# Optimization experiments

Hardware: AMD Instinct MI355X
Metric: run time of the kernel (lower is better)

## Reference

```python
import jax, jax.numpy as jnp
import numpy as np

N_CLASSES = 256
PER_CLASS = 128
N_SUPPORT = 5
N_QUERY = PER_CLASS - N_SUPPORT  # 123
N_VIEW = 2
D = 384
N = N_CLASSES * PER_CLASS  # 32768


def setup_inputs() -> dict:
    key = jax.random.key(0)
    k1, k2 = jax.random.split(key, 2)
    reps = jax.random.normal(k1, (N, N_VIEW, D), dtype=jnp.float32)
    # block-sorted labels: class c occupies rows [c*PER_CLASS, (c+1)*PER_CLASS)
    labels = (jnp.arange(N, dtype=jnp.int32) // PER_CLASS).astype(jnp.int32)
    return {"reps": reps, "labels": labels}


def reference(reps, labels):
    # labels are block-sorted per class, so the original's
    # labels.eq(c).nonzero()[:n_support] / [n_support:] gathers are static reshapes.
    reps_r = reps.reshape(N_CLASSES, PER_CLASS, N_VIEW, D)
    # class-mean prototypes over the support set: [C, V, D]
    prototypes = reps_r[:, :N_SUPPORT].mean(axis=1)
    # query samples: [C*N_QUERY, V, D]
    queries = reps_r[:, N_SUPPORT:].reshape(N_CLASSES * N_QUERY, N_VIEW, D)

    x2 = jnp.sum(queries * queries, axis=-1)            # [n, V]
    y2 = jnp.sum(prototypes * prototypes, axis=-1)      # [m, V]
    xy = jnp.einsum('nvd,mvd->nmv', queries, prototypes)  # [n, m, V]
    dists = x2[:, None, :] + y2[None, :, :] - 2.0 * xy

    # log_softmax over the prototype (class) axis
    log_p_y = jax.nn.log_softmax(-dists, axis=1)
    log_p_y = log_p_y.reshape(N_CLASSES, N_QUERY, N_CLASSES, N_VIEW)

    # gather the true-class log-prob for each query / view
    cls = jnp.arange(N_CLASSES)
    correct = log_p_y[cls, :, cls, :]  # [C, N_QUERY, V]
    loss = -correct.mean()
    return loss
```

## Files before the change

### kernel.cpp

```cpp
#include <hip/hip_runtime.h>
#include <hip/hip_bf16.h>
#include <math.h>

#define NCLS 256
#define PER_CLASS 128
#define NSUP 5
#define NQRY 123
#define NVIEW 2
#define DD 384
#define NQ_TOT (NCLS * NQRY)
#define BM 128
#define BK 32
#define NKT (DD / BK)
#define QS 40

typedef __attribute__((ext_vector_type(8))) short short8;
typedef __attribute__((ext_vector_type(4))) float floatx4;

union FragU { uint4 u; short8 s; };
union PkU { __hip_bfloat162 b2; unsigned int u; };

__device__ __forceinline__ unsigned int cvt2bf(float lo, float hi) {
    PkU p;
    p.b2 = __float22bfloat162_rn(make_float2(lo, hi));
    return p.u;
}

#define BARRIER() asm volatile("s_waitcnt lgkmcnt(0)\n\ts_barrier" ::: "memory")

__global__ __launch_bounds__(384) void proto_kernel(const float* __restrict__ reps,
                                                    ushort* __restrict__ pbf,
                                                    float* __restrict__ y2) {
    __shared__ float wp[6];
    const int b = blockIdx.x;
    const int c = b & 255, v = b >> 8;
    const int d = threadIdx.x;
    const float* p = reps + ((size_t)(c * PER_CLASS) * NVIEW + v) * DD + d;
    float s = 0.f;
#pragma unroll
    for (int k = 0; k < NSUP; ++k) s += p[(size_t)k * NVIEW * DD];
    s *= 0.2f;
    __hip_bfloat16 h = __float2bfloat16(s);
    pbf[(size_t)b * DD + d] = *reinterpret_cast<ushort*>(&h);
    float q = s * s;
#pragma unroll
    for (int o = 1; o < 64; o <<= 1) q += __shfl_xor(q, o);
    if ((d & 63) == 0) wp[d >> 6] = q;
    __syncthreads();
    if (d == 0) y2[b] = wp[0] + wp[1] + wp[2] + wp[3] + wp[4] + wp[5];
}

__global__ __launch_bounds__(256, 2) void main_kernel(const float* __restrict__ reps,
                                                      const ushort* __restrict__ pbf,
                                                      const float* __restrict__ y2g,
                                                      float* __restrict__ out) {
    __shared__ ushort q_lds[2][BM * QS];
    __shared__ ushort p_lds[2][NCLS * QS];
    __shared__ float pmx[BM][2];
    __shared__ float pse[BM][2];
    __shared__ float wred[8];

    const int t = threadIdx.x;
    const int v = blockIdx.y;
    const int q0 = blockIdx.x * BM;
    const int wave = t >> 6;
    const int lane = t & 63;
    const int col = lane & 15;
    const int quad = lane >> 4;
    const int wm = wave >> 1;
    const int wn = wave & 1;

    const int sq = t >> 1;
    const int h16 = (t & 1) * 16;
    const int nq = q0 + sq;
    const float* qsrc = reps +
        (size_t)((nq / NQRY) * PER_CLASS + NSUP + (nq % NQRY)) * (NVIEW * DD) + v * DD + h16;
    const ushort* psrc = pbf + (size_t)(v * NCLS + t) * DD;

    floatx4 acc[4][8];
#pragma unroll
    for (int mt = 0; mt < 4; ++mt)
#pragma unroll
        for (int nt = 0; nt < 8; ++nt) acc[mt][nt] = (floatx4)0.f;

    float4 qf[4];
    uint4 pl[4];

#define LOADT(kt)                                                                  \
    do {                                                                           \
        _Pragma("unroll") for (int i = 0; i < 4; ++i)                              \
            qf[i] = *(const float4*)(qsrc + (kt) * BK + i * 4);                    \
        _Pragma("unroll") for (int i = 0; i < 4; ++i)                              \
            pl[i] = *((const uint4*)(psrc + (kt) * BK) + i);                       \
    } while (0)

#define STAGE(b)                                                                   \
    do {                                                                           \
        uint4 qw0, qw1;                                                            \
        qw0.x = cvt2bf(qf[0].x, qf[0].y); qw0.y = cvt2bf(qf[0].z, qf[0].w);        \
        qw0.z = cvt2bf(qf[1].x, qf[1].y); qw0.w = cvt2bf(qf[1].z, qf[1].w);        \
        qw1.x = cvt2bf(qf[2].x, qf[2].y); qw1.y = cvt2bf(qf[2].z, qf[2].w);        \
        qw1.z = cvt2bf(qf[3].x, qf[3].y); qw1.w = cvt2bf(qf[3].z, qf[3].w);        \
        *(uint4*)&q_lds[b][sq * QS + h16] = qw0;                                   \
        *(uint4*)&q_lds[b][sq * QS + h16 + 8] = qw1;                               \
        _Pragma("unroll") for (int i = 0; i < 4; ++i)                              \
            *(uint4*)&p_lds[b][t * QS + i * 8] = pl[i];                            \
    } while (0)

#define COMPUTE(b)                                                                 \
    do {                                                                           \
        short8 af[4];                                                              \
        _Pragma("unroll") for (int mt = 0; mt < 4; ++mt) {                         \
            FragU f;                                                               \
            f.u = *(const uint4*)&q_lds[b][(wm * 64 + mt * 16 + col) * QS + quad * 8]; \
            af[mt] = f.s;                                                          \
        }                                                                          \
        _Pragma("unroll") for (int nt = 0; nt < 8; ++nt) {                         \
            FragU bb;                                                              \
            bb.u = *(const uint4*)&p_lds[b][(wn * 128 + nt * 16 + col) * QS + quad * 8]; \
            _Pragma("unroll") for (int mt = 0; mt < 4; ++mt)                       \
                acc[mt][nt] = __builtin_amdgcn_mfma_f32_16x16x32_bf16(af[mt], bb.s, acc[mt][nt], 0, 0, 0); \
        }                                                                          \
    } while (0)

    LOADT(0);
    STAGE(0);
    LOADT(1);
    BARRIER();
#pragma unroll
    for (int kt = 0; kt < NKT; ++kt) {
        COMPUTE(kt & 1);
        if (kt < NKT - 1) {
            STAGE((kt + 1) & 1);
            if (kt < NKT - 2) LOADT(kt + 2);
            BARRIER();
        }
    }

    float y2c[8];
#pragma unroll
    for (int nt = 0; nt < 8; ++nt) y2c[nt] = y2g[v * NCLS + wn * 128 + nt * 16 + col];

    float corr = 0.f;
#pragma unroll
    for (int mt = 0; mt < 4; ++mt) {
#pragma unroll
        for (int r = 0; r < 4; ++r) {
            const int qloc = wm * 64 + mt * 16 + quad * 4 + r;
            const int n = q0 + qloc;
            const int cn = n / NQRY;
            float s[8];
            float mx = -1e30f;
#pragma unroll
            for (int nt = 0; nt < 8; ++nt) {
                s[nt] = 2.f * acc[mt][nt][r] - y2c[nt];
                mx = fmaxf(mx, s[nt]);
                if (cn == wn * 128 + nt * 16 + col) corr += s[nt];
            }
#pragma unroll
            for (int o = 1; o < 16; o <<= 1) mx = fmaxf(mx, __shfl_xor(mx, o));
            float e = 0.f;
#pragma unroll
            for (int nt = 0; nt < 8; ++nt) e += __expf(s[nt] - mx);
#pragma unroll
            for (int o = 1; o < 16; o <<= 1) e += __shfl_xor(e, o);
            if (col == 0) { pmx[qloc][wn] = mx; pse[qloc][wn] = e; }
        }
    }
#pragma unroll
    for (int o = 1; o < 64; o <<= 1) corr += __shfl_xor(corr, o);
    if (lane == 0) wred[wave] = corr;
    __syncthreads();

    float lval = 0.f;
    if (t < BM) {
        float m0 = pmx[t][0], m1 = pmx[t][1];
        float M = fmaxf(m0, m1);
        float E = pse[t][0] * __expf(m0 - M) + pse[t][1] * __expf(m1 - M);
        lval = M + __logf(E);
    }
#pragma unroll
    for (int o = 1; o < 64; o <<= 1) lval += __shfl_xor(lval, o);
    if (lane == 0) wred[4 + wave] = lval;
    __syncthreads();

    if (t == 0) {
        float tot = (wred[4] + wred[5] + wred[6] + wred[7]) -
                    (wred[0] + wred[1] + wred[2] + wred[3]);
        atomicAdd(out, tot * (1.f / (float)(NQ_TOT * NVIEW)));
    }
}

extern "C" void kernel_launch(void* const* d_in, const int* in_sizes, int n_in,
                              void* d_out, int out_size, void* d_ws, size_t ws_size,
                              hipStream_t stream) {
    const float* reps = (const float*)d_in[0];
    float* ws = (float*)d_ws;
    ushort* pbf = (ushort*)ws;
    float* y2 = (float*)(pbf + NVIEW * NCLS * DD);
    float* out = (float*)d_out;

    hipMemsetAsync(out, 0, sizeof(float), stream);
    proto_kernel<<<dim3(NVIEW * NCLS), dim3(DD), 0, stream>>>(reps, pbf, y2);
    main_kernel<<<dim3(NQ_TOT / BM, NVIEW), dim3(256), 0, stream>>>(reps, pbf, y2, out);
}
```

Before: 164.9 us.

## Load prototype tiles via global_load_lds with XOR swizzle and deeper Q prefetch

Prototype bf16 tiles now go straight from global memory into LDS through global_load_lds, skipping the register round trip. They use an XOR-swizzled unpadded layout to avoid bank conflicts on MFMA fragment reads. Query loads are double-buffered in registers two tiles ahead, with explicit vmcnt waits. The separate memset is folded into the prototype kernel to remove a launch. The cost is more complex synchronisation and tighter correctness requirements on the swizzle and wait counts.

```diff
diff --git a/kernel.cpp b/kernel.cpp
--- a/kernel.cpp
+++ b/kernel.cpp
@@ -13,6 +13,7 @@
 #define BK 32
 #define NKT (DD / BK)
 #define QS 40
+#define PS 32
 
 typedef __attribute__((ext_vector_type(8))) short short8;
 typedef __attribute__((ext_vector_type(4))) float floatx4;
@@ -26,15 +27,24 @@
     return p.u;
 }
 
+__device__ __forceinline__ void gll16(const ushort* g, ushort* l) {
+    __builtin_amdgcn_global_load_lds(
+        (const __attribute__((address_space(1))) unsigned int*)g,
+        (__attribute__((address_space(3))) unsigned int*)l, 16, 0, 0);
+}
+
 #define BARRIER() asm volatile("s_waitcnt lgkmcnt(0)\n\ts_barrier" ::: "memory")
+#define WAITVM(n) asm volatile("s_waitcnt vmcnt(" #n ")" ::: "memory")
 
 __global__ __launch_bounds__(384) void proto_kernel(const float* __restrict__ reps,
                                                     ushort* __restrict__ pbf,
-                                                    float* __restrict__ y2) {
+                                                    float* __restrict__ y2,
+                                                    float* __restrict__ out) {
     __shared__ float wp[6];
     const int b = blockIdx.x;
     const int c = b & 255, v = b >> 8;
     const int d = threadIdx.x;
+    if (b == 0 && d == 0) out[0] = 0.f;
     const float* p = reps + ((size_t)(c * PER_CLASS) * NVIEW + v) * DD + d;
     float s = 0.f;
 #pragma unroll
@@ -55,7 +65,7 @@
                                                       const float* __restrict__ y2g,
                                                       float* __restrict__ out) {
     __shared__ ushort q_lds[2][BM * QS];
-    __shared__ ushort p_lds[2][NCLS * QS];
+    __shared__ ushort p_lds[2][NCLS * PS];
     __shared__ float pmx[BM][2];
     __shared__ float pse[BM][2];
     __shared__ float wred[8];
@@ -75,7 +85,15 @@
     const int nq = q0 + sq;
     const float* qsrc = reps +
         (size_t)((nq / NQRY) * PER_CLASS + NSUP + (nq % NQRY)) * (NVIEW * DD) + v * DD + h16;
-    const ushort* psrc = pbf + (size_t)(v * NCLS + t) * DD;
+
+    const ushort* psrc = pbf + (size_t)(v * NCLS + wave * 64 + (lane >> 2)) * DD
+                             + (((lane & 3) ^ ((lane >> 3) & 3)) << 3);
+
+    const int sP = (col >> 1) & 3;
+    int boff[8];
+#pragma unroll
+    for (int nt = 0; nt < 8; ++nt)
+        boff[nt] = (wn * 128 + nt * 16 + col) * PS + ((quad ^ sP) << 3);
 
     floatx4 acc[4][8];
 #pragma unroll
@@ -83,28 +101,30 @@
 #pragma unroll
         for (int nt = 0; nt < 8; ++nt) acc[mt][nt] = (floatx4)0.f;
 
-    float4 qf[4];
-    uint4 pl[4];
-
-#define LOADT(kt)                                                                  \
+    float4 qfA[4], qfB[4];
+
+#define LOADQ(kt, R)                                                               \
     do {                                                                           \
         _Pragma("unroll") for (int i = 0; i < 4; ++i)                              \
-            qf[i] = *(const float4*)(qsrc + (kt) * BK + i * 4);                    \
+            R[i] = *(const float4*)(qsrc + (kt) * BK + i * 4);                     \
+    } while (0)
+
+#define GLLP(kt, b)                                                                \
+    do {                                                                           \
         _Pragma("unroll") for (int i = 0; i < 4; ++i)                              \
-            pl[i] = *((const uint4*)(psrc + (kt) * BK) + i);                       \
-    } while (0)
-
-#define STAGE(b)                                                                   \
-    do {                                                                           \
-        uint4 qw0, qw1;                                                            \
-        qw0.x = cvt2bf(qf[0].x, qf[0].y); qw0.y = cvt2bf(qf[0].z, qf[0].w);        \
-        qw0.z = cvt2bf(qf[1].x, qf[1].y); qw0.w = cvt2bf(qf[1].z, qf[1].w);        \
-        qw1.x = cvt2bf(qf[2].x, qf[2].y); qw1.y = cvt2bf(qf[2].z, qf[2].w);        \
-        qw1.z = cvt2bf(qf[3].x, qf[3].y); qw1.w = cvt2bf(qf[3].z, qf[3].w);        \
-        *(uint4*)&q_lds[b][sq * QS + h16] = qw0;                                   \
-        *(uint4*)&q_lds[b][sq * QS + h16 + 8] = qw1;                               \
-        _Pragma("unroll") for (int i = 0; i < 4; ++i)                              \
-            *(uint4*)&p_lds[b][t * QS + i * 8] = pl[i];                            \
+            gll16(psrc + i * (16 * DD) + (kt) * BK,                                \
+                  &p_lds[b][wave * 2048 + i * 512]);                               \
+    } while (0)
+
+#define STAGEQ(b, R)                                                               \
+    do {                                                                           \
+        uint4 w0, w1;                                                              \
+        w0.x = cvt2bf(R[0].x, R[0].y); w0.y = cvt2bf(R[0].z, R[0].w);              \
+        w0.z = cvt2bf(R[1].x, R[1].y); w0.w = cvt2bf(R[1].z, R[1].w);              \
+        w1.x = cvt2bf(R[2].x, R[2].y); w1.y = cvt2bf(R[2].z, R[2].w);              \
+        w1.z = cvt2bf(R[3].x, R[3].y); w1.w = cvt2bf(R[3].z, R[3].w);              \
+        *(uint4*)&q_lds[b][sq * QS + h16] = w0;                                    \
+        *(uint4*)&q_lds[b][sq * QS + h16 + 8] = w1;                                \
     } while (0)
 
 #define COMPUTE(b)                                                                 \
@@ -117,24 +137,32 @@
         }                                                                          \
         _Pragma("unroll") for (int nt = 0; nt < 8; ++nt) {                         \
             FragU bb;                                                              \
-            bb.u = *(const uint4*)&p_lds[b][(wn * 128 + nt * 16 + col) * QS + quad * 8]; \
+            bb.u = *(const uint4*)&p_lds[b][boff[nt]];                             \
             _Pragma("unroll") for (int mt = 0; mt < 4; ++mt)                       \
                 acc[mt][nt] = __builtin_amdgcn_mfma_f32_16x16x32_bf16(af[mt], bb.s, acc[mt][nt], 0, 0, 0); \
         }                                                                          \
     } while (0)
 
-    LOADT(0);
-    STAGE(0);
-    LOADT(1);
+    LOADQ(0, qfA); GLLP(0, 0);
+    LOADQ(1, qfB); GLLP(1, 1);
+    WAITVM(8);
+    STAGEQ(0, qfA);
     BARRIER();
+
 #pragma unroll
     for (int kt = 0; kt < NKT; ++kt) {
         COMPUTE(kt & 1);
-        if (kt < NKT - 1) {
-            STAGE((kt + 1) & 1);
-            if (kt < NKT - 2) LOADT(kt + 2);
-            BARRIER();
+        if (kt == NKT - 1) break;
+        BARRIER();
+        if (kt + 2 < NKT) {
+            if ((kt & 1) == 0) { LOADQ(kt + 2, qfA); } else { LOADQ(kt + 2, qfB); }
+            GLLP(kt + 2, kt & 1);
+            WAITVM(8);
+        } else {
+            WAITVM(0);
         }
+        if ((kt & 1) == 0) STAGEQ(1, qfB); else STAGEQ(0, qfA);
+        BARRIER();
     }
 
     float y2c[8];
@@ -200,7 +228,6 @@
     float* y2 = (float*)(pbf + NVIEW * NCLS * DD);
     float* out = (float*)d_out;
 
-    hipMemsetAsync(out, 0, sizeof(float), stream);
-    proto_kernel<<<dim3(NVIEW * NCLS), dim3(DD), 0, stream>>>(reps, pbf, y2);
+    proto_kernel<<<dim3(NVIEW * NCLS), dim3(DD), 0, stream>>>(reps, pbf, y2, out);
     main_kernel<<<dim3(NQ_TOT / BM, NVIEW), dim3(256), 0, stream>>>(reps, pbf, y2, out);
 }
```

Result: no change. 162.4 us (-1.5%).

## Drop LDS staging; each wave loads fragments straight from global into registers

Applied to the files above, without the earlier changes.

The main kernel no longer stages query and prototype tiles through LDS with barriers. Each of 8 waves owns 16 query rows and all 256 classes, and loads A and B MFMA fragments directly from global memory (prototypes from L2) with double-buffered registers. The cross-wave log-sum-exp merge and the host memset are also removed, with the output zeroed inside proto_kernel instead. The trade is that each wave now rereads the full prototype matrix from cache, and 32 uint4 buffer registers per lane raise register pressure.

```diff
diff --git a/kernel.cpp b/kernel.cpp
--- a/kernel.cpp
+++ b/kernel.cpp
@@ -9,10 +9,10 @@
 #define NVIEW 2
 #define DD 384
 #define NQ_TOT (NCLS * NQRY)
-#define BM 128
 #define BK 32
 #define NKT (DD / BK)
-#define QS 40
+#define WROWS 16
+#define BROWS 128
 
 typedef __attribute__((ext_vector_type(8))) short short8;
 typedef __attribute__((ext_vector_type(4))) float floatx4;
@@ -26,15 +26,15 @@
     return p.u;
 }
 
-#define BARRIER() asm volatile("s_waitcnt lgkmcnt(0)\n\ts_barrier" ::: "memory")
-
 __global__ __launch_bounds__(384) void proto_kernel(const float* __restrict__ reps,
                                                     ushort* __restrict__ pbf,
-                                                    float* __restrict__ y2) {
+                                                    float* __restrict__ y2,
+                                                    float* __restrict__ out) {
     __shared__ float wp[6];
     const int b = blockIdx.x;
     const int c = b & 255, v = b >> 8;
     const int d = threadIdx.x;
+    if (b == 0 && d == 0) out[0] = 0.f;
     const float* p = reps + ((size_t)(c * PER_CLASS) * NVIEW + v) * DD + d;
     float s = 0.f;
 #pragma unroll
@@ -50,143 +50,111 @@
     if (d == 0) y2[b] = wp[0] + wp[1] + wp[2] + wp[3] + wp[4] + wp[5];
 }
 
-__global__ __launch_bounds__(256, 2) void main_kernel(const float* __restrict__ reps,
+__global__ __launch_bounds__(512, 2) void main_kernel(const float* __restrict__ reps,
                                                       const ushort* __restrict__ pbf,
                                                       const float* __restrict__ y2g,
                                                       float* __restrict__ out) {
-    __shared__ ushort q_lds[2][BM * QS];
-    __shared__ ushort p_lds[2][NCLS * QS];
-    __shared__ float pmx[BM][2];
-    __shared__ float pse[BM][2];
-    __shared__ float wred[8];
+    __shared__ float wred[16];
 
     const int t = threadIdx.x;
     const int v = blockIdx.y;
-    const int q0 = blockIdx.x * BM;
     const int wave = t >> 6;
     const int lane = t & 63;
     const int col = lane & 15;
     const int quad = lane >> 4;
-    const int wm = wave >> 1;
-    const int wn = wave & 1;
+    const int q0 = blockIdx.x * BROWS + wave * WROWS;
 
-    const int sq = t >> 1;
-    const int h16 = (t & 1) * 16;
-    const int nq = q0 + sq;
+    const int nq = q0 + col;
     const float* qsrc = reps +
-        (size_t)((nq / NQRY) * PER_CLASS + NSUP + (nq % NQRY)) * (NVIEW * DD) + v * DD + h16;
-    const ushort* psrc = pbf + (size_t)(v * NCLS + t) * DD;
+        (size_t)((nq / NQRY) * PER_CLASS + NSUP + (nq % NQRY)) * (NVIEW * DD) +
+        v * DD + quad * 8;
+    const ushort* psrc = pbf + (size_t)(v * NCLS + col) * DD + quad * 8;
 
-    floatx4 acc[4][8];
+    floatx4 acc[16];
 #pragma unroll
-    for (int mt = 0; mt < 4; ++mt)
-#pragma unroll
-        for (int nt = 0; nt < 8; ++nt) acc[mt][nt] = (floatx4)0.f;
+    for (int nt = 0; nt < 16; ++nt) acc[nt] = (floatx4)0.f;
 
-    float4 qf[4];
-    uint4 pl[4];
+    float4 qf[2][2];
+    uint4 pb_[2][16];
 
-#define LOADT(kt)                                                                  \
+#define LOADA(kt, b)                                                               \
     do {                                                                           \
-        _Pragma("unroll") for (int i = 0; i < 4; ++i)                              \
-            qf[i] = *(const float4*)(qsrc + (kt) * BK + i * 4);                    \
-        _Pragma("unroll") for (int i = 0; i < 4; ++i)                              \
-            pl[i] = *((const uint4*)(psrc + (kt) * BK) + i);                       \
+        qf[b][0] = *(const float4*)(qsrc + (kt) * BK);                             \
+        qf[b][1] = *(const float4*)(qsrc + (kt) * BK + 4);                         \
     } while (0)
 
-#define STAGE(b)                                                                   \
+#define LOADB(kt, b)                                                               \
     do {                                                                           \
-        uint4 qw0, qw1;                                                            \
-        qw0.x = cvt2bf(qf[0].x, qf[0].y); qw0.y = cvt2bf(qf[0].z, qf[0].w);        \
-        qw0.z = cvt2bf(qf[1].x, qf[1].y); qw0.w = cvt2bf(qf[1].z, qf[1].w);        \
-        qw1.x = cvt2bf(qf[2].x, qf[2].y); qw1.y = cvt2bf(qf[2].z, qf[2].w);        \
-        qw1.z = cvt2bf(qf[3].x, qf[3].y); qw1.w = cvt2bf(qf[3].z, qf[3].w);        \
-        *(uint4*)&q_lds[b][sq * QS + h16] = qw0;                                   \
-        *(uint4*)&q_lds[b][sq * QS + h16 + 8] = qw1;                               \
-        _Pragma("unroll") for (int i = 0; i < 4; ++i)                              \
-            *(uint4*)&p_lds[b][t * QS + i * 8] = pl[i];                            \
+        _Pragma("unroll") for (int nt = 0; nt < 16; ++nt)                          \
+            pb_[b][nt] = *(const uint4*)(psrc + (size_t)nt * 16 * DD + (kt) * BK); \
     } while (0)
 
 #define COMPUTE(b)                                                                 \
     do {                                                                           \
-        short8 af[4];                                                              \
-        _Pragma("unroll") for (int mt = 0; mt < 4; ++mt) {                         \
-            FragU f;                                                               \
-            f.u = *(const uint4*)&q_lds[b][(wm * 64 + mt * 16 + col) * QS + quad * 8]; \
-            af[mt] = f.s;                                                          \
-        }                                                                          \
-        _Pragma("unroll") for (int nt = 0; nt < 8; ++nt) {                         \
+        FragU f;                                                                   \
+        f.u.x = cvt2bf(qf[b][0].x, qf[b][0].y);                                    \
+        f.u.y = cvt2bf(qf[b][0].z, qf[b][0].w);                                    \
+        f.u.z = cvt2bf(qf[b][1].x, qf[b][1].y);                                    \
+        f.u.w = cvt2bf(qf[b][1].z, qf[b][1].w);                                    \
+        _Pragma("unroll") for (int nt = 0; nt < 16; ++nt) {                        \
             FragU bb;                                                              \
-            bb.u = *(const uint4*)&p_lds[b][(wn * 128 + nt * 16 + col) * QS + quad * 8]; \
-            _Pragma("unroll") for (int mt = 0; mt < 4; ++mt)                       \
-                acc[mt][nt] = __builtin_amdgcn_mfma_f32_16x16x32_bf16(af[mt], bb.s, acc[mt][nt], 0, 0, 0); \
+            bb.u = pb_[b][nt];                                                     \
+            acc[nt] = __builtin_amdgcn_mfma_f32_16x16x32_bf16(f.s, bb.s, acc[nt], 0, 0, 0); \
         }                                                                          \
     } while (0)
 
-    LOADT(0);
-    STAGE(0);
-    LOADT(1);
-    BARRIER();
+    LOADA(0, 0); LOADB(0, 0);
+    LOADA(1, 1); LOADB(1, 1);
+
 #pragma unroll
     for (int kt = 0; kt < NKT; ++kt) {
         COMPUTE(kt & 1);
-        if (kt < NKT - 1) {
-            STAGE((kt + 1) & 1);
-            if (kt < NKT - 2) LOADT(kt + 2);
-            BARRIER();
+        if (kt + 2 < NKT) {
+            LOADA(kt + 2, kt & 1);
+            LOADB(kt + 2, kt & 1);
         }
     }
 
-    float y2c[8];
+    float y2c[16];
 #pragma unroll
-    for (int nt = 0; nt < 8; ++nt) y2c[nt] = y2g[v * NCLS + wn * 128 + nt * 16 + col];
+    for (int nt = 0; nt < 16; ++nt) y2c[nt] = y2g[v * NCLS + nt * 16 + col];
 
     float corr = 0.f;
+    float lsum = 0.f;
 #pragma unroll
-    for (int mt = 0; mt < 4; ++mt) {
+    for (int r = 0; r < 4; ++r) {
+        const int n = q0 + quad * 4 + r;
+        const int cn = n / NQRY;
+        float s[16];
+        float mx = -1e30f;
 #pragma unroll
-        for (int r = 0; r < 4; ++r) {
-            const int qloc = wm * 64 + mt * 16 + quad * 4 + r;
-            const int n = q0 + qloc;
-            const int cn = n / NQRY;
-            float s[8];
-            float mx = -1e30f;
+        for (int nt = 0; nt < 16; ++nt) {
+            s[nt] = 2.f * acc[nt][r] - y2c[nt];
+            mx = fmaxf(mx, s[nt]);
+            if (cn == nt * 16 + col) corr += s[nt];
+        }
 #pragma unroll
-            for (int nt = 0; nt < 8; ++nt) {
-                s[nt] = 2.f * acc[mt][nt][r] - y2c[nt];
-                mx = fmaxf(mx, s[nt]);
-                if (cn == wn * 128 + nt * 16 + col) corr += s[nt];
-            }
+        for (int o = 1; o < 16; o <<= 1) mx = fmaxf(mx, __shfl_xor(mx, o));
+        float e = 0.f;
 #pragma unroll
-            for (int o = 1; o < 16; o <<= 1) mx = fmaxf(mx, __shfl_xor(mx, o));
-            float e = 0.f;
+        for (int nt = 0; nt < 16; ++nt) e += __expf(s[nt] - mx);
 #pragma unroll
-            for (int nt = 0; nt < 8; ++nt) e += __expf(s[nt] - mx);
-#pragma unroll
-            for (int o = 1; o < 16; o <<= 1) e += __shfl_xor(e, o);
-            if (col == 0) { pmx[qloc][wn] = mx; pse[qloc][wn] = e; }
-        }
+        for (int o = 1; o < 16; o <<= 1) e += __shfl_xor(e, o);
+        if (col == 0) lsum += mx + __logf(e);
     }
 #pragma unroll
-    for (int o = 1; o < 64; o <<= 1) corr += __shfl_xor(corr, o);
-    if (lane == 0) wred[wave] = corr;
-    __syncthreads();
-
-    float lval = 0.f;
-    if (t < BM) {
-        float m0 = pmx[t][0], m1 = pmx[t][1];
-        float M = fmaxf(m0, m1);
-        float E = pse[t][0] * __expf(m0 - M) + pse[t][1] * __expf(m1 - M);
-        lval = M + __logf(E);
+    for (int o = 1; o < 64; o <<= 1) {
+        lsum += __shfl_xor(lsum, o);
+        corr += __shfl_xor(corr, o);
     }
-#pragma unroll
-    for (int o = 1; o < 64; o <<= 1) lval += __shfl_xor(lval, o);
-    if (lane == 0) wred[4 + wave] = lval;
+    if (lane == 0) { wred[wave] = lsum; wred[8 + wave] = corr; }
     __syncthreads();
 
     if (t == 0) {
-        float tot = (wred[4] + wred[5] + wred[6] + wred[7]) -
-                    (wred[0] + wred[1] + wred[2] + wred[3]);
+        float tot = (wred[0] + wred[1] + wred[2] + wred[3] +
+                     wred[4] + wred[5] + wred[6] + wred[7]) -
+                    (wred[8] + wred[9] + wred[10] + wred[11] +
+                     wred[12] + wred[13] + wred[14] + wred[15]);
         atomicAdd(out, tot * (1.f / (float)(NQ_TOT * NVIEW)));
     }
 }
@@ -200,7 +168,6 @@
     float* y2 = (float*)(pbf + NVIEW * NCLS * DD);
     float* out = (float*)d_out;
 
-    hipMemsetAsync(out, 0, sizeof(float), stream);
-    proto_kernel<<<dim3(NVIEW * NCLS), dim3(DD), 0, stream>>>(reps, pbf, y2);
-    main_kernel<<<dim3(NQ_TOT / BM, NVIEW), dim3(256), 0, stream>>>(reps, pbf, y2, out);
+    proto_kernel<<<dim3(NVIEW * NCLS), dim3(DD), 0, stream>>>(reps, pbf, y2, out);
+    main_kernel<<<dim3(NQ_TOT / BROWS, NVIEW), dim3(512), 0, stream>>>(reps, pbf, y2, out);
 }
```

Measured after the change: 233.1 us. 41.4% more time.
